# Kernel tuning notes

Hardware: AMD Instinct MI355X
Metric: run time of the kernel (lower is better)

The kernel has to match this reference:

```python
import jax, jax.numpy as jnp
import numpy as np

N = 50000
E = 800000
IN_C, HID, OUT_C = 512, 256, 128


def gcn_conv(x, edge_index, W, b, num_nodes):
    # PyG GCNConv: add self-loops, symmetric normalization, linear-then-aggregate.
    h = x @ W  # [N, out]
    src = jnp.concatenate([edge_index[0], jnp.arange(num_nodes)])
    dst = jnp.concatenate([edge_index[1], jnp.arange(num_nodes)])
    ones = jnp.ones(src.shape[0], dtype=x.dtype)
    deg = jax.ops.segment_sum(ones, dst, num_segments=num_nodes)  # in-degree incl. self-loop
    dinv = jax.lax.rsqrt(deg)  # deg >= 1 thanks to self-loops
    norm = dinv[src] * dinv[dst]  # [E+N]
    msg = h[src] * norm[:, None]  # gather + scale
    out = jax.ops.segment_sum(msg, dst, num_segments=num_nodes)  # scatter-add
    return out + b


def setup_inputs() -> dict:
    key = jax.random.key(0)
    k_x, k_e, k_w1, k_b1, k_w2, k_b2 = jax.random.split(key, 6)
    x = jax.random.normal(k_x, (N, IN_C), dtype=jnp.float32)
    edge_index = jax.random.randint(k_e, (2, E), 0, N, dtype=jnp.int64)
    s1 = 1.0 / np.sqrt(IN_C)
    s2 = 1.0 / np.sqrt(HID)
    W1 = jax.random.uniform(k_w1, (IN_C, HID), jnp.float32, -s1, s1)
    b1 = jax.random.uniform(k_b1, (HID,), jnp.float32, -s1, s1)
    W2 = jax.random.uniform(k_w2, (HID, OUT_C), jnp.float32, -s2, s2)
    b2 = jax.random.uniform(k_b2, (OUT_C,), jnp.float32, -s2, s2)
    return {"x": x, "edge_index": edge_index, "W1": W1, "b1": b1, "W2": W2, "b2": b2}


def reference(x, edge_index, W1, b1, W2, b2):
    h = gcn_conv(x, edge_index, W1, b1, N)
    h = jax.nn.relu(h)
    # dropout in eval mode == identity
    return gcn_conv(h, edge_index, W2, b2, N)
```

## Files before the change

### kernel.cpp

```cpp
#include <hip/hip_runtime.h>
#include <stdint.h>

typedef __bf16 bf16_t;
typedef bf16_t bf16x8 __attribute__((ext_vector_type(8)));
typedef bf16_t bf16x4 __attribute__((ext_vector_type(4)));
typedef bf16_t bf16x2 __attribute__((ext_vector_type(2)));
typedef float  f32x4  __attribute__((ext_vector_type(4)));

typedef __attribute__((address_space(3))) void* as3p;
typedef const __attribute__((address_space(1))) void* as1p;

#define IN_C 512
#define HID  256
#define OUTC 128

__global__ void k_prep(const float* __restrict__ x, const float* __restrict__ W1,
                       const float* __restrict__ W2, const void* __restrict__ ei,
                       int* __restrict__ flag, int* __restrict__ cnt,
                       bf16_t* __restrict__ Xb, bf16_t* __restrict__ W1t,
                       bf16_t* __restrict__ W2t, int n, int mpad) {
  int t = blockIdx.x * blockDim.x + threadIdx.x;
  const int NC = mpad * 64;
  if (t < NC) {
    int r = t >> 6, c8 = t & 63;
    bf16x8 o;
    if (r < n) {
      const float4* px = (const float4*)(x + (size_t)r * IN_C);
      float4 a = px[c8 * 2];
      float4 b = px[c8 * 2 + 1];
      o[0] = (bf16_t)a.x; o[1] = (bf16_t)a.y; o[2] = (bf16_t)a.z; o[3] = (bf16_t)a.w;
      o[4] = (bf16_t)b.x; o[5] = (bf16_t)b.y; o[6] = (bf16_t)b.z; o[7] = (bf16_t)b.w;
    } else {
      for (int i = 0; i < 8; ++i) o[i] = (bf16_t)0.0f;
    }
    *(bf16x8*)(Xb + (size_t)r * IN_C + c8 * 8) = o;
    return;
  }
  int u = t - NC;
  if (u < IN_C * HID) {
    W1t[(size_t)(u & 255) * IN_C + (u >> 8)] = (bf16_t)W1[u];
    return;
  }
  u -= IN_C * HID;
  if (u < HID * OUTC) {
    W2t[(size_t)(u & 127) * HID + (u >> 7)] = (bf16_t)W2[u];
    return;
  }
  u -= HID * OUTC;
  if (u < n) {
    cnt[u] = 0;
    return;
  }
  if (u == n) {
    const long long* p = (const long long*)ei;
    int ok = 1;
    for (int i = 0; i < 64; ++i) {
      long long v = p[i];
      if (v < 0 || v >= n) ok = 0;
    }
    *flag = ok;
  }
}

__global__ void k_hist(const void* __restrict__ ei, const int* __restrict__ flag,
                       int* __restrict__ cnt, int E) {
  int e = blockIdx.x * blockDim.x + threadIdx.x;
  if (e >= E) return;
  int d;
  if (*flag) d = (int)((const long long*)ei)[(size_t)E + e];
  else       d = ((const int*)ei)[E + e];
  atomicAdd(&cnt[d], 1);
}

__global__ void k_scan1(const int* __restrict__ cnt, int* __restrict__ ex,
                        int* __restrict__ part, float* __restrict__ dinv, int n) {
  __shared__ int sh[256];
  int i = blockIdx.x * 256 + threadIdx.x;
  int v = (i < n) ? cnt[i] : 0;
  if (i < n) dinv[i] = rsqrtf((float)v + 1.0f);
  sh[threadIdx.x] = v;
  __syncthreads();
  int val = v;
  for (int off = 1; off < 256; off <<= 1) {
    int t = (threadIdx.x >= off) ? sh[threadIdx.x - off] : 0;
    __syncthreads();
    val += t;
    sh[threadIdx.x] = val;
    __syncthreads();
  }
  if (i < n) ex[i] = val - v;
  if (threadIdx.x == 255) part[blockIdx.x] = val;
}

__global__ void k_scan23(int* __restrict__ rs, const int* __restrict__ part,
                         int* __restrict__ cur, int n, int Etot) {
  __shared__ int sh[256];
  const int b = blockIdx.x, t = threadIdx.x;
  int p = 0;
  for (int j = t; j < b; j += 256) p += part[j];
  sh[t] = p;
  __syncthreads();
  for (int off = 128; off > 0; off >>= 1) {
    if (t < off) sh[t] += sh[t + off];
    __syncthreads();
  }
  int base = sh[0];
  int i = b * 256 + t;
  if (i < n) {
    int r = rs[i] + base;
    rs[i] = r;
    cur[i] = r;
  }
  if (i == 0) rs[n] = Etot;
}

__global__ void k_fill(const void* __restrict__ ei, const int* __restrict__ flag,
                       int* __restrict__ cur, int2* __restrict__ csrw,
                       const float* __restrict__ dinv, int E) {
  int e = blockIdx.x * blockDim.x + threadIdx.x;
  if (e >= E) return;
  int s, d;
  if (*flag) {
    const long long* p = (const long long*)ei;
    s = (int)p[e];
    d = (int)p[(size_t)E + e];
  } else {
    const int* p = (const int*)ei;
    s = p[e];
    d = p[E + e];
  }
  int pos = atomicAdd(&cur[d], 1);
  int2 v;
  v.x = s;
  v.y = __float_as_int(dinv[s]);
  csrw[pos] = v;
}

__global__ __launch_bounds__(256, 3) void k_gemm(const bf16_t* __restrict__ A,
                                                 const bf16_t* __restrict__ Bt,
                                                 bf16_t* __restrict__ C,
                                                 int Kdim, int Ncols) {
  __shared__ bf16_t As[128 * 32];
  __shared__ bf16_t Bs[128 * 32];
  const int bm = blockIdx.x, bn = blockIdx.y;
  const int tid = threadIdx.x;
  const int wave = tid >> 6, lane = tid & 63;
  const int wm = (wave >> 1) * 64, wn = (wave & 1) * 64;
  const int quad = lane >> 4, l16 = lane & 15;

  const size_t abase = (size_t)bm * 128 * Kdim;
  const size_t bbase = (size_t)bn * 128 * Kdim;

  f32x4 acc[4][4];
#pragma unroll
  for (int i = 0; i < 4; ++i)
#pragma unroll
    for (int j = 0; j < 4; ++j)
#pragma unroll
      for (int r = 0; r < 4; ++r) acc[i][j][r] = 0.0f;

  for (int kk = 0; kk < Kdim; kk += 32) {
#pragma unroll
    for (int i = 0; i < 2; ++i) {
      int g = i * 256 + tid;
      int row = g >> 2, col = (g & 3) * 8;
      const bf16_t* ga = A + abase + (size_t)row * Kdim + kk + col;
      __builtin_amdgcn_global_load_lds((as1p)ga,
                                       (as3p)(&As[(i * 256 + wave * 64) * 8]), 16, 0, 0);
      const bf16_t* gb = Bt + bbase + (size_t)row * Kdim + kk + col;
      __builtin_amdgcn_global_load_lds((as1p)gb,
                                       (as3p)(&Bs[(i * 256 + wave * 64) * 8]), 16, 0, 0);
    }
    __syncthreads();
    bf16x8 af[4], bf[4];
#pragma unroll
    for (int i = 0; i < 4; ++i)
      af[i] = *(const bf16x8*)(&As[(wm + i * 16 + l16) * 32 + quad * 8]);
#pragma unroll
    for (int j = 0; j < 4; ++j)
      bf[j] = *(const bf16x8*)(&Bs[(wn + j * 16 + l16) * 32 + quad * 8]);
#pragma unroll
    for (int i = 0; i < 4; ++i)
#pragma unroll
      for (int j = 0; j < 4; ++j)
        acc[i][j] = __builtin_amdgcn_mfma_f32_16x16x32_bf16(af[i], bf[j], acc[i][j], 0, 0, 0);
    __syncthreads();
  }

#pragma unroll
  for (int i = 0; i < 4; ++i) {
#pragma unroll
    for (int j = 0; j < 4; ++j) {
      int col = bn * 128 + wn + j * 16 + l16;
      int row0 = bm * 128 + wm + i * 16 + quad * 4;
#pragma unroll
      for (int r = 0; r < 4; ++r)
        C[(size_t)(row0 + r) * Ncols + col] = (bf16_t)acc[i][j][r];
    }
  }
}

__global__ void k_agg_l1(const bf16_t* __restrict__ H, const int* __restrict__ rs,
                         const int2* __restrict__ csrw, const float* __restrict__ dinv,
                         const float* __restrict__ b1, bf16_t* __restrict__ R,
                         int n, int mpad) {
  int d = blockIdx.x * 4 + (threadIdx.x >> 6);
  if (d >= mpad) return;
  int lane = threadIdx.x & 63;
  if (d >= n) {
    bf16x4 z;
    z[0] = (bf16_t)0.0f; z[1] = (bf16_t)0.0f; z[2] = (bf16_t)0.0f; z[3] = (bf16_t)0.0f;
    *(bf16x4*)(R + (size_t)d * HID + lane * 4) = z;
    return;
  }
  int e0 = rs[d], e1 = rs[d + 1];
  float acc[4][4];
  for (int k = 0; k < 4; ++k)
    for (int c = 0; c < 4; ++c) acc[k][c] = 0.f;
  int e = e0;
  for (; e + 8 <= e1; e += 8) {
    int2 cw[8];
    bf16x4 h[8];
#pragma unroll
    for (int u = 0; u < 8; ++u) cw[u] = csrw[e + u];
#pragma unroll
    for (int u = 0; u < 8; ++u)
      h[u] = *(const bf16x4*)(H + (size_t)cw[u].x * HID + lane * 4);
#pragma unroll
    for (int u = 0; u < 8; ++u) {
      float w = __int_as_float(cw[u].y);
#pragma unroll
      for (int c = 0; c < 4; ++c) acc[u & 3][c] += w * (float)h[u][c];
    }
  }
  for (; e < e1; ++e) {
    int2 cw = csrw[e];
    float w = __int_as_float(cw.y);
    bf16x4 hx = *(const bf16x4*)(H + (size_t)cw.x * HID + lane * 4);
#pragma unroll
    for (int c = 0; c < 4; ++c) acc[0][c] += w * (float)hx[c];
  }
  float dd = dinv[d];
  float dv2 = dd * dd;
  bf16x4 hs = *(const bf16x4*)(H + (size_t)d * HID + lane * 4);
  float4 bb = ((const float4*)b1)[lane];
  float a0 = (acc[0][0] + acc[1][0]) + (acc[2][0] + acc[3][0]);
  float a1 = (acc[0][1] + acc[1][1]) + (acc[2][1] + acc[3][1]);
  float a2 = (acc[0][2] + acc[1][2]) + (acc[2][2] + acc[3][2]);
  float a3 = (acc[0][3] + acc[1][3]) + (acc[2][3] + acc[3][3]);
  float v0 = fmaxf(a0 * dd + dv2 * (float)hs[0] + bb.x, 0.f);
  float v1 = fmaxf(a1 * dd + dv2 * (float)hs[1] + bb.y, 0.f);
  float v2 = fmaxf(a2 * dd + dv2 * (float)hs[2] + bb.z, 0.f);
  float v3 = fmaxf(a3 * dd + dv2 * (float)hs[3] + bb.w, 0.f);
  bf16x4 o;
  o[0] = (bf16_t)v0; o[1] = (bf16_t)v1; o[2] = (bf16_t)v2; o[3] = (bf16_t)v3;
  *(bf16x4*)(R + (size_t)d * HID + lane * 4) = o;
}

__global__ void k_agg_l2(const bf16_t* __restrict__ H, const int* __restrict__ rs,
                         const int2* __restrict__ csrw, const float* __restrict__ dinv,
                         const float* __restrict__ b2, float* __restrict__ out, int n) {
  int d = blockIdx.x * 4 + (threadIdx.x >> 6);
  if (d >= n) return;
  int lane = threadIdx.x & 63;
  int e0 = rs[d], e1 = rs[d + 1];
  float acc[4][2];
  for (int k = 0; k < 4; ++k) { acc[k][0] = 0.f; acc[k][1] = 0.f; }
  int e = e0;
  for (; e + 8 <= e1; e += 8) {
    int2 cw[8];
    bf16x2 h[8];
#pragma unroll
    for (int u = 0; u < 8; ++u) cw[u] = csrw[e + u];
#pragma unroll
    for (int u = 0; u < 8; ++u)
      h[u] = *(const bf16x2*)(H + (size_t)cw[u].x * OUTC + lane * 2);
#pragma unroll
    for (int u = 0; u < 8; ++u) {
      float w = __int_as_float(cw[u].y);
      acc[u & 3][0] += w * (float)h[u][0];
      acc[u & 3][1] += w * (float)h[u][1];
    }
  }
  for (; e < e1; ++e) {
    int2 cw = csrw[e];
    float w = __int_as_float(cw.y);
    bf16x2 hx = *(const bf16x2*)(H + (size_t)cw.x * OUTC + lane * 2);
    acc[0][0] += w * (float)hx[0];
    acc[0][1] += w * (float)hx[1];
  }
  float a0 = (acc[0][0] + acc[1][0]) + (acc[2][0] + acc[3][0]);
  float a1 = (acc[0][1] + acc[1][1]) + (acc[2][1] + acc[3][1]);
  float dd = dinv[d];
  float dv2 = dd * dd;
  bf16x2 hs = *(const bf16x2*)(H + (size_t)d * OUTC + lane * 2);
  float2 bb = ((const float2*)b2)[lane];
  float2 o;
  o.x = a0 * dd + dv2 * (float)hs[0] + bb.x;
  o.y = a1 * dd + dv2 * (float)hs[1] + bb.y;
  ((float2*)(out + (size_t)d * OUTC))[lane] = o;
}

extern "C" void kernel_launch(void* const* d_in, const int* in_sizes, int n_in,
                              void* d_out, int out_size, void* d_ws, size_t ws_size,
                              hipStream_t stream) {
  const float* x  = (const float*)d_in[0];
  const void*  ei = d_in[1];
  const float* W1 = (const float*)d_in[2];
  const float* b1 = (const float*)d_in[3];
  const float* W2 = (const float*)d_in[4];
  const float* b2 = (const float*)d_in[5];

  const int n = in_sizes[0] / IN_C;
  const int E = in_sizes[1] / 2;
  const int mpad = (n + 127) & ~127;

  char* w = (char*)d_ws;
  size_t off = 0;
  auto alloc = [&](size_t bytes) -> void* {
    void* p = w + off;
    off = (off + bytes + 255) & ~(size_t)255;
    return p;
  };

  int*    flag = (int*)alloc(4);
  int*    cnt  = (int*)alloc((size_t)n * 4);
  float*  dinv = (float*)alloc((size_t)n * 4);
  int*    rs   = (int*)alloc((size_t)(n + 1) * 4);
  int*    cur  = (int*)alloc((size_t)n * 4);
  int*    part = (int*)alloc(1024);
  int2*   csrw = (int2*)alloc((size_t)E * 8);
  bf16_t* Xb   = (bf16_t*)alloc((size_t)mpad * IN_C * 2);
  bf16_t* W1t  = (bf16_t*)alloc((size_t)HID * IN_C * 2);
  bf16_t* W2t  = (bf16_t*)alloc((size_t)OUTC * HID * 2);
  bf16_t* H1b  = (bf16_t*)alloc((size_t)mpad * HID * 2);
  bf16_t* R1b  = (bf16_t*)alloc((size_t)mpad * HID * 2);
  bf16_t* H2b  = (bf16_t*)alloc((size_t)mpad * OUTC * 2);
  (void)ws_size; (void)n_in; (void)out_size;

  const int nb = (n + 255) / 256;
  const int prepT = mpad * 64 + IN_C * HID + HID * OUTC + n + 1;

  k_prep<<<(prepT + 255) / 256, 256, 0, stream>>>(x, W1, W2, ei, flag, cnt,
                                                  Xb, W1t, W2t, n, mpad);
  k_hist<<<(E + 255) / 256, 256, 0, stream>>>(ei, flag, cnt, E);
  k_scan1<<<nb, 256, 0, stream>>>(cnt, rs, part, dinv, n);
  k_scan23<<<nb, 256, 0, stream>>>(rs, part, cur, n, E);
  k_fill<<<(E + 255) / 256, 256, 0, stream>>>(ei, flag, cur, csrw, dinv, E);

  k_gemm<<<dim3(mpad / 128, HID / 128), 256, 0, stream>>>(Xb, W1t, H1b, IN_C, HID);
  k_agg_l1<<<(mpad + 3) / 4, 256, 0, stream>>>(H1b, rs, csrw, dinv, b1, R1b, n, mpad);
  k_gemm<<<dim3(mpad / 128, OUTC / 128), 256, 0, stream>>>(R1b, W2t, H2b, HID, OUTC);
  k_agg_l2<<<(n + 3) / 4, 256, 0, stream>>>(H2b, rs, csrw, dinv, b2, (float*)d_out, n);
}
```

Measured before the change: 397.0 us.

## Fuse fp32-to-bf16 conversion into layer-1 GEMM, merge scans, shrink CSR entries

The separate pass that converts x to bf16 is removed. The layer-1 GEMM now reads fp32 x directly, converts it in registers and stages it into padded LDS tiles, with each block covering the full 256 output columns. The two scan kernels become one, where each block recomputes its prefix by summing the preceding counts directly. CSR entries drop from (src, weight) pairs to plain src indices, and the aggregation kernels gather dinv[src] per edge instead. The trade-offs are redundant prefix summation work, extra random dinv loads in aggregation, and loss of the async global-to-LDS loads in GEMM1 along with lower occupancy.

```diff
diff --git a/kernel.cpp b/kernel.cpp
--- a/kernel.cpp
+++ b/kernel.cpp
@@ -14,29 +14,18 @@
 #define HID  256
 #define OUTC 128
 
-__global__ void k_prep(const float* __restrict__ x, const float* __restrict__ W1,
-                       const float* __restrict__ W2, const void* __restrict__ ei,
-                       int* __restrict__ flag, int* __restrict__ cnt,
-                       bf16_t* __restrict__ Xb, bf16_t* __restrict__ W1t,
-                       bf16_t* __restrict__ W2t, int n, int mpad) {
-  int t = blockIdx.x * blockDim.x + threadIdx.x;
-  const int NC = mpad * 64;
-  if (t < NC) {
-    int r = t >> 6, c8 = t & 63;
-    bf16x8 o;
-    if (r < n) {
-      const float4* px = (const float4*)(x + (size_t)r * IN_C);
-      float4 a = px[c8 * 2];
-      float4 b = px[c8 * 2 + 1];
-      o[0] = (bf16_t)a.x; o[1] = (bf16_t)a.y; o[2] = (bf16_t)a.z; o[3] = (bf16_t)a.w;
-      o[4] = (bf16_t)b.x; o[5] = (bf16_t)b.y; o[6] = (bf16_t)b.z; o[7] = (bf16_t)b.w;
-    } else {
-      for (int i = 0; i < 8; ++i) o[i] = (bf16_t)0.0f;
-    }
-    *(bf16x8*)(Xb + (size_t)r * IN_C + c8 * 8) = o;
-    return;
-  }
-  int u = t - NC;
+__device__ inline bf16x8 cvt8(float4 a, float4 b) {
+  bf16x8 o;
+  o[0] = (bf16_t)a.x; o[1] = (bf16_t)a.y; o[2] = (bf16_t)a.z; o[3] = (bf16_t)a.w;
+  o[4] = (bf16_t)b.x; o[5] = (bf16_t)b.y; o[6] = (bf16_t)b.z; o[7] = (bf16_t)b.w;
+  return o;
+}
+
+__global__ void k_prep(const float* __restrict__ W1, const float* __restrict__ W2,
+                       const void* __restrict__ ei, int* __restrict__ flag,
+                       int* __restrict__ cnt, bf16_t* __restrict__ W1t,
+                       bf16_t* __restrict__ W2t, int n) {
+  int u = blockIdx.x * blockDim.x + threadIdx.x;
   if (u < IN_C * HID) {
     W1t[(size_t)(u & 255) * IN_C + (u >> 8)] = (bf16_t)W1[u];
     return;
@@ -72,32 +61,13 @@
   atomicAdd(&cnt[d], 1);
 }
 
-__global__ void k_scan1(const int* __restrict__ cnt, int* __restrict__ ex,
-                        int* __restrict__ part, float* __restrict__ dinv, int n) {
-  __shared__ int sh[256];
-  int i = blockIdx.x * 256 + threadIdx.x;
-  int v = (i < n) ? cnt[i] : 0;
-  if (i < n) dinv[i] = rsqrtf((float)v + 1.0f);
-  sh[threadIdx.x] = v;
-  __syncthreads();
-  int val = v;
-  for (int off = 1; off < 256; off <<= 1) {
-    int t = (threadIdx.x >= off) ? sh[threadIdx.x - off] : 0;
-    __syncthreads();
-    val += t;
-    sh[threadIdx.x] = val;
-    __syncthreads();
-  }
-  if (i < n) ex[i] = val - v;
-  if (threadIdx.x == 255) part[blockIdx.x] = val;
-}
-
-__global__ void k_scan23(int* __restrict__ rs, const int* __restrict__ part,
-                         int* __restrict__ cur, int n, int Etot) {
+__global__ void k_scan(const int* __restrict__ cnt, int* __restrict__ rs,
+                       int* __restrict__ cur, float* __restrict__ dinv,
+                       int n, int Etot) {
   __shared__ int sh[256];
   const int b = blockIdx.x, t = threadIdx.x;
   int p = 0;
-  for (int j = t; j < b; j += 256) p += part[j];
+  for (int j = t; j < b * 256; j += 256) p += cnt[j];
   sh[t] = p;
   __syncthreads();
   for (int off = 128; off > 0; off >>= 1) {
@@ -105,9 +75,22 @@
     __syncthreads();
   }
   int base = sh[0];
+  __syncthreads();
   int i = b * 256 + t;
+  int v = (i < n) ? cnt[i] : 0;
+  if (i < n) dinv[i] = rsqrtf((float)v + 1.0f);
+  sh[t] = v;
+  __syncthreads();
+  int val = v;
+  for (int off = 1; off < 256; off <<= 1) {
+    int tt = (t >= off) ? sh[t - off] : 0;
+    __syncthreads();
+    val += tt;
+    sh[t] = val;
+    __syncthreads();
+  }
   if (i < n) {
-    int r = rs[i] + base;
+    int r = base + val - v;
     rs[i] = r;
     cur[i] = r;
   }
@@ -115,8 +98,7 @@
 }
 
 __global__ void k_fill(const void* __restrict__ ei, const int* __restrict__ flag,
-                       int* __restrict__ cur, int2* __restrict__ csrw,
-                       const float* __restrict__ dinv, int E) {
+                       int* __restrict__ cur, int* __restrict__ csr, int E) {
   int e = blockIdx.x * blockDim.x + threadIdx.x;
   if (e >= E) return;
   int s, d;
@@ -130,26 +112,91 @@
     d = p[E + e];
   }
   int pos = atomicAdd(&cur[d], 1);
-  int2 v;
-  v.x = s;
-  v.y = __float_as_int(dinv[s]);
-  csrw[pos] = v;
-}
-
-__global__ __launch_bounds__(256, 3) void k_gemm(const bf16_t* __restrict__ A,
-                                                 const bf16_t* __restrict__ Bt,
-                                                 bf16_t* __restrict__ C,
-                                                 int Kdim, int Ncols) {
+  csr[pos] = s;
+}
+
+__global__ __launch_bounds__(256, 2) void k_gemm1(const float* __restrict__ x,
+                                                  const bf16_t* __restrict__ W1t,
+                                                  bf16_t* __restrict__ C, int n) {
+  __shared__ bf16_t As[128 * 40];
+  __shared__ bf16_t Bs[256 * 40];
+  const int bm = blockIdx.x;
+  const int tid = threadIdx.x;
+  const int wave = tid >> 6, lane = tid & 63;
+  const int wm = (wave >> 1) * 64, wn = (wave & 1) * 128;
+  const int quad = lane >> 4, l16 = lane & 15;
+  const int arow = tid >> 1, acol = (tid & 1) * 16;
+  const int grow = bm * 128 + arow;
+  const bool av = grow < n;
+  const float* ap = x + (size_t)grow * IN_C + acol;
+  const bf16_t* bp = W1t + (size_t)tid * IN_C;
+
+  f32x4 acc[4][8];
+#pragma unroll
+  for (int i = 0; i < 4; ++i)
+#pragma unroll
+    for (int j = 0; j < 8; ++j)
+#pragma unroll
+      for (int r = 0; r < 4; ++r) acc[i][j][r] = 0.0f;
+
+  for (int kk = 0; kk < IN_C; kk += 32) {
+    float4 z = {0, 0, 0, 0};
+    float4 a0 = av ? *(const float4*)(ap + kk)      : z;
+    float4 a1 = av ? *(const float4*)(ap + kk + 4)  : z;
+    float4 a2 = av ? *(const float4*)(ap + kk + 8)  : z;
+    float4 a3 = av ? *(const float4*)(ap + kk + 12) : z;
+    bf16x8 vb0 = *(const bf16x8*)(bp + kk);
+    bf16x8 vb1 = *(const bf16x8*)(bp + kk + 8);
+    bf16x8 vb2 = *(const bf16x8*)(bp + kk + 16);
+    bf16x8 vb3 = *(const bf16x8*)(bp + kk + 24);
+    bf16x8 va0 = cvt8(a0, a1);
+    bf16x8 va1 = cvt8(a2, a3);
+    __syncthreads();
+    *(bf16x8*)(&As[arow * 40 + acol]) = va0;
+    *(bf16x8*)(&As[arow * 40 + acol + 8]) = va1;
+    *(bf16x8*)(&Bs[tid * 40]) = vb0;
+    *(bf16x8*)(&Bs[tid * 40 + 8]) = vb1;
+    *(bf16x8*)(&Bs[tid * 40 + 16]) = vb2;
+    *(bf16x8*)(&Bs[tid * 40 + 24]) = vb3;
+    __syncthreads();
+    bf16x8 af[4], bf[8];
+#pragma unroll
+    for (int i = 0; i < 4; ++i)
+      af[i] = *(const bf16x8*)(&As[(wm + i * 16 + l16) * 40 + quad * 8]);
+#pragma unroll
+    for (int j = 0; j < 8; ++j)
+      bf[j] = *(const bf16x8*)(&Bs[(wn + j * 16 + l16) * 40 + quad * 8]);
+#pragma unroll
+    for (int i = 0; i < 4; ++i)
+#pragma unroll
+      for (int j = 0; j < 8; ++j)
+        acc[i][j] = __builtin_amdgcn_mfma_f32_16x16x32_bf16(af[i], bf[j], acc[i][j], 0, 0, 0);
+  }
+
+#pragma unroll
+  for (int i = 0; i < 4; ++i) {
+#pragma unroll
+    for (int j = 0; j < 8; ++j) {
+      int col = wn + j * 16 + l16;
+      int row0 = bm * 128 + wm + i * 16 + quad * 4;
+#pragma unroll
+      for (int r = 0; r < 4; ++r)
+        C[(size_t)(row0 + r) * HID + col] = (bf16_t)acc[i][j][r];
+    }
+  }
+}
+
+__global__ __launch_bounds__(256, 3) void k_gemm2(const bf16_t* __restrict__ A,
+                                                  const bf16_t* __restrict__ Bt,
+                                                  bf16_t* __restrict__ C) {
   __shared__ bf16_t As[128 * 32];
   __shared__ bf16_t Bs[128 * 32];
-  const int bm = blockIdx.x, bn = blockIdx.y;
+  const int bm = blockIdx.x;
   const int tid = threadIdx.x;
   const int wave = tid >> 6, lane = tid & 63;
   const int wm = (wave >> 1) * 64, wn = (wave & 1) * 64;
   const int quad = lane >> 4, l16 = lane & 15;
-
-  const size_t abase = (size_t)bm * 128 * Kdim;
-  const size_t bbase = (size_t)bn * 128 * Kdim;
+  const size_t abase = (size_t)bm * 128 * HID;
 
   f32x4 acc[4][4];
 #pragma unroll
@@ -159,15 +206,15 @@
 #pragma unroll
       for (int r = 0; r < 4; ++r) acc[i][j][r] = 0.0f;
 
-  for (int kk = 0; kk < Kdim; kk += 32) {
+  for (int kk = 0; kk < HID; kk += 32) {
 #pragma unroll
     for (int i = 0; i < 2; ++i) {
       int g = i * 256 + tid;
       int row = g >> 2, col = (g & 3) * 8;
-      const bf16_t* ga = A + abase + (size_t)row * Kdim + kk + col;
+      const bf16_t* ga = A + abase + (size_t)row * HID + kk + col;
       __builtin_amdgcn_global_load_lds((as1p)ga,
                                        (as3p)(&As[(i * 256 + wave * 64) * 8]), 16, 0, 0);
-      const bf16_t* gb = Bt + bbase + (size_t)row * Kdim + kk + col;
+      const bf16_t* gb = Bt + (size_t)row * HID + kk + col;
       __builtin_amdgcn_global_load_lds((as1p)gb,
                                        (as3p)(&Bs[(i * 256 + wave * 64) * 8]), 16, 0, 0);
     }
@@ -191,17 +238,17 @@
   for (int i = 0; i < 4; ++i) {
 #pragma unroll
     for (int j = 0; j < 4; ++j) {
-      int col = bn * 128 + wn + j * 16 + l16;
+      int col = wn + j * 16 + l16;
       int row0 = bm * 128 + wm + i * 16 + quad * 4;
 #pragma unroll
       for (int r = 0; r < 4; ++r)
-        C[(size_t)(row0 + r) * Ncols + col] = (bf16_t)acc[i][j][r];
+        C[(size_t)(row0 + r) * OUTC + col] = (bf16_t)acc[i][j][r];
     }
   }
 }
 
 __global__ void k_agg_l1(const bf16_t* __restrict__ H, const int* __restrict__ rs,
-                         const int2* __restrict__ csrw, const float* __restrict__ dinv,
+                         const int* __restrict__ csr, const float* __restrict__ dinv,
                          const float* __restrict__ b1, bf16_t* __restrict__ R,
                          int n, int mpad) {
   int d = blockIdx.x * 4 + (threadIdx.x >> 6);
@@ -219,26 +266,27 @@
     for (int c = 0; c < 4; ++c) acc[k][c] = 0.f;
   int e = e0;
   for (; e + 8 <= e1; e += 8) {
-    int2 cw[8];
+    int s[8];
+    float w[8];
     bf16x4 h[8];
 #pragma unroll
-    for (int u = 0; u < 8; ++u) cw[u] = csrw[e + u];
+    for (int u = 0; u < 8; ++u) s[u] = csr[e + u];
+#pragma unroll
+    for (int u = 0; u < 8; ++u) w[u] = dinv[s[u]];
 #pragma unroll
     for (int u = 0; u < 8; ++u)
-      h[u] = *(const bf16x4*)(H + (size_t)cw[u].x * HID + lane * 4);
-#pragma unroll
-    for (int u = 0; u < 8; ++u) {
-      float w = __int_as_float(cw[u].y);
-#pragma unroll
-      for (int c = 0; c < 4; ++c) acc[u & 3][c] += w * (float)h[u][c];
-    }
+      h[u] = *(const bf16x4*)(H + (size_t)s[u] * HID + lane * 4);
+#pragma unroll
+    for (int u = 0; u < 8; ++u)
+#pragma unroll
+      for (int c = 0; c < 4; ++c) acc[u & 3][c] += w[u] * (float)h[u][c];
   }
   for (; e < e1; ++e) {
-    int2 cw = csrw[e];
-    float w = __int_as_float(cw.y);
-    bf16x4 hx = *(const bf16x4*)(H + (size_t)cw.x * HID + lane * 4);
-#pragma unroll
-    for (int c = 0; c < 4; ++c) acc[0][c] += w * (float)hx[c];
+    int sx = csr[e];
+    float wx = dinv[sx];
+    bf16x4 hx = *(const bf16x4*)(H + (size_t)sx * HID + lane * 4);
+#pragma unroll
+    for (int c = 0; c < 4; ++c) acc[0][c] += wx * (float)hx[c];
   }
   float dd = dinv[d];
   float dv2 = dd * dd;
@@ -258,7 +306,7 @@
 }
 
 __global__ void k_agg_l2(const bf16_t* __restrict__ H, const int* __restrict__ rs,
-                         const int2* __restrict__ csrw, const float* __restrict__ dinv,
+                         const int* __restrict__ csr, const float* __restrict__ dinv,
                          const float* __restrict__ b2, float* __restrict__ out, int n) {
   int d = blockIdx.x * 4 + (threadIdx.x >> 6);
   if (d >= n) return;
@@ -268,26 +316,28 @@
   for (int k = 0; k < 4; ++k) { acc[k][0] = 0.f; acc[k][1] = 0.f; }
   int e = e0;
   for (; e + 8 <= e1; e += 8) {
-    int2 cw[8];
+    int s[8];
+    float w[8];
     bf16x2 h[8];
 #pragma unroll
-    for (int u = 0; u < 8; ++u) cw[u] = csrw[e + u];
+    for (int u = 0; u < 8; ++u) s[u] = csr[e + u];
+#pragma unroll
+    for (int u = 0; u < 8; ++u) w[u] = dinv[s[u]];
 #pragma unroll
     for (int u = 0; u < 8; ++u)
-      h[u] = *(const bf16x2*)(H + (size_t)cw[u].x * OUTC + lane * 2);
+      h[u] = *(const bf16x2*)(H + (size_t)s[u] * OUTC + lane * 2);
 #pragma unroll
     for (int u = 0; u < 8; ++u) {
-      float w = __int_as_float(cw[u].y);
-      acc[u & 3][0] += w * (float)h[u][0];
-      acc[u & 3][1] += w * (float)h[u][1];
+      acc[u & 3][0] += w[u] * (float)h[u][0];
+      acc[u & 3][1] += w[u] * (float)h[u][1];
     }
   }
   for (; e < e1; ++e) {
-    int2 cw = csrw[e];
-    float w = __int_as_float(cw.y);
-    bf16x2 hx = *(const bf16x2*)(H + (size_t)cw.x * OUTC + lane * 2);
-    acc[0][0] += w * (float)hx[0];
-    acc[0][1] += w * (float)hx[1];
+    int sx = csr[e];
+    float wx = dinv[sx];
+    bf16x2 hx = *(const bf16x2*)(H + (size_t)sx * OUTC + lane * 2);
+    acc[0][0] += wx * (float)hx[0];
+    acc[0][1] += wx * (float)hx[1];
   }
   float a0 = (acc[0][0] + acc[1][0]) + (acc[2][0] + acc[3][0]);
   float a1 = (acc[0][1] + acc[1][1]) + (acc[2][1] + acc[3][1]);
@@ -328,9 +378,7 @@
   float*  dinv = (float*)alloc((size_t)n * 4);
   int*    rs   = (int*)alloc((size_t)(n + 1) * 4);
   int*    cur  = (int*)alloc((size_t)n * 4);
-  int*    part = (int*)alloc(1024);
-  int2*   csrw = (int2*)alloc((size_t)E * 8);
-  bf16_t* Xb   = (bf16_t*)alloc((size_t)mpad * IN_C * 2);
+  int*    csr  = (int*)alloc((size_t)E * 4);
   bf16_t* W1t  = (bf16_t*)alloc((size_t)HID * IN_C * 2);
   bf16_t* W2t  = (bf16_t*)alloc((size_t)OUTC * HID * 2);
   bf16_t* H1b  = (bf16_t*)alloc((size_t)mpad * HID * 2);
@@ -339,17 +387,15 @@
   (void)ws_size; (void)n_in; (void)out_size;
 
   const int nb = (n + 255) / 256;
-  const int prepT = mpad * 64 + IN_C * HID + HID * OUTC + n + 1;
-
-  k_prep<<<(prepT + 255) / 256, 256, 0, stream>>>(x, W1, W2, ei, flag, cnt,
-                                                  Xb, W1t, W2t, n, mpad);
+  const int prepT = IN_C * HID + HID * OUTC + n + 1;
+
+  k_prep<<<(prepT + 255) / 256, 256, 0, stream>>>(W1, W2, ei, flag, cnt, W1t, W2t, n);
   k_hist<<<(E + 255) / 256, 256, 0, stream>>>(ei, flag, cnt, E);
-  k_scan1<<<nb, 256, 0, stream>>>(cnt, rs, part, dinv, n);
-  k_scan23<<<nb, 256, 0, stream>>>(rs, part, cur, n, E);
-  k_fill<<<(E + 255) / 256, 256, 0, stream>>>(ei, flag, cur, csrw, dinv, E);
-
-  k_gemm<<<dim3(mpad / 128, HID / 128), 256, 0, stream>>>(Xb, W1t, H1b, IN_C, HID);
-  k_agg_l1<<<(mpad + 3) / 4, 256, 0, stream>>>(H1b, rs, csrw, dinv, b1, R1b, n, mpad);
-  k_gemm<<<dim3(mpad / 128, OUTC / 128), 256, 0, stream>>>(R1b, W2t, H2b, HID, OUTC);
-  k_agg_l2<<<(n + 3) / 4, 256, 0, stream>>>(H2b, rs, csrw, dinv, b2, (float*)d_out, n);
-}
+  k_scan<<<nb, 256, 0, stream>>>(cnt, rs, cur, dinv, n, E);
+  k_fill<<<(E + 255) / 256, 256, 0, stream>>>(ei, flag, cur, csr, E);
+
+  k_gemm1<<<mpad / 128, 256, 0, stream>>>(x, W1t, H1b, n);
+  k_agg_l1<<<(mpad + 3) / 4, 256, 0, stream>>>(H1b, rs, csr, dinv, b1, R1b, n, mpad);
+  k_gemm2<<<mpad / 128, 256, 0, stream>>>(R1b, W2t, H2b);
+  k_agg_l2<<<(n + 3) / 4, 256, 0, stream>>>(H2b, rs, csr, dinv, b2, (float*)d_out, n);
+}
```

New measurement: 454.9 us. +14.6%, slower.

## Merge scan kernels and store source-only CSR, gathering dinv in aggregation

Applied to the files above, without the earlier changes.

Folds the two-pass prefix scan into a single kernel in which each block recomputes its base offset by summing all preceding counts directly. The CSR now stores only source indices (int) rather than (src, dinv) pairs, which halves CSR bytes and lets the fill kernel skip the dinv gather. The aggregation kernels then gather dinv[s] per edge themselves. In exchange, each scan block does work that grows with its index (quadratic total reads of cnt), and aggregation picks up an extra dependent random load per edge.

```diff
diff --git a/kernel.cpp b/kernel.cpp
--- a/kernel.cpp
+++ b/kernel.cpp
@@ -72,32 +72,13 @@
   atomicAdd(&cnt[d], 1);
 }
 
-__global__ void k_scan1(const int* __restrict__ cnt, int* __restrict__ ex,
-                        int* __restrict__ part, float* __restrict__ dinv, int n) {
-  __shared__ int sh[256];
-  int i = blockIdx.x * 256 + threadIdx.x;
-  int v = (i < n) ? cnt[i] : 0;
-  if (i < n) dinv[i] = rsqrtf((float)v + 1.0f);
-  sh[threadIdx.x] = v;
-  __syncthreads();
-  int val = v;
-  for (int off = 1; off < 256; off <<= 1) {
-    int t = (threadIdx.x >= off) ? sh[threadIdx.x - off] : 0;
-    __syncthreads();
-    val += t;
-    sh[threadIdx.x] = val;
-    __syncthreads();
-  }
-  if (i < n) ex[i] = val - v;
-  if (threadIdx.x == 255) part[blockIdx.x] = val;
-}
-
-__global__ void k_scan23(int* __restrict__ rs, const int* __restrict__ part,
-                         int* __restrict__ cur, int n, int Etot) {
+__global__ void k_scan(const int* __restrict__ cnt, int* __restrict__ rs,
+                       int* __restrict__ cur, float* __restrict__ dinv,
+                       int n, int Etot) {
   __shared__ int sh[256];
   const int b = blockIdx.x, t = threadIdx.x;
   int p = 0;
-  for (int j = t; j < b; j += 256) p += part[j];
+  for (int j = t; j < b * 256; j += 256) p += cnt[j];
   sh[t] = p;
   __syncthreads();
   for (int off = 128; off > 0; off >>= 1) {
@@ -105,9 +86,22 @@
     __syncthreads();
   }
   int base = sh[0];
+  __syncthreads();
   int i = b * 256 + t;
+  int v = (i < n) ? cnt[i] : 0;
+  if (i < n) dinv[i] = rsqrtf((float)v + 1.0f);
+  sh[t] = v;
+  __syncthreads();
+  int val = v;
+  for (int off = 1; off < 256; off <<= 1) {
+    int tt = (t >= off) ? sh[t - off] : 0;
+    __syncthreads();
+    val += tt;
+    sh[t] = val;
+    __syncthreads();
+  }
   if (i < n) {
-    int r = rs[i] + base;
+    int r = base + val - v;
     rs[i] = r;
     cur[i] = r;
   }
@@ -115,8 +109,7 @@
 }
 
 __global__ void k_fill(const void* __restrict__ ei, const int* __restrict__ flag,
-                       int* __restrict__ cur, int2* __restrict__ csrw,
-                       const float* __restrict__ dinv, int E) {
+                       int* __restrict__ cur, int* __restrict__ csr, int E) {
   int e = blockIdx.x * blockDim.x + threadIdx.x;
   if (e >= E) return;
   int s, d;
@@ -130,10 +123,7 @@
     d = p[E + e];
   }
   int pos = atomicAdd(&cur[d], 1);
-  int2 v;
-  v.x = s;
-  v.y = __float_as_int(dinv[s]);
-  csrw[pos] = v;
+  csr[pos] = s;
 }
 
 __global__ __launch_bounds__(256, 3) void k_gemm(const bf16_t* __restrict__ A,
@@ -201,7 +191,7 @@
 }
 
 __global__ void k_agg_l1(const bf16_t* __restrict__ H, const int* __restrict__ rs,
-                         const int2* __restrict__ csrw, const float* __restrict__ dinv,
+                         const int* __restrict__ csr, const float* __restrict__ dinv,
                          const float* __restrict__ b1, bf16_t* __restrict__ R,
                          int n, int mpad) {
   int d = blockIdx.x * 4 + (threadIdx.x >> 6);
@@ -219,26 +209,27 @@
     for (int c = 0; c < 4; ++c) acc[k][c] = 0.f;
   int e = e0;
   for (; e + 8 <= e1; e += 8) {
-    int2 cw[8];
+    int s[8];
+    float w[8];
     bf16x4 h[8];
 #pragma unroll
-    for (int u = 0; u < 8; ++u) cw[u] = csrw[e + u];
+    for (int u = 0; u < 8; ++u) s[u] = csr[e + u];
+#pragma unroll
+    for (int u = 0; u < 8; ++u) w[u] = dinv[s[u]];
 #pragma unroll
     for (int u = 0; u < 8; ++u)
-      h[u] = *(const bf16x4*)(H + (size_t)cw[u].x * HID + lane * 4);
-#pragma unroll
-    for (int u = 0; u < 8; ++u) {
-      float w = __int_as_float(cw[u].y);
-#pragma unroll
-      for (int c = 0; c < 4; ++c) acc[u & 3][c] += w * (float)h[u][c];
-    }
+      h[u] = *(const bf16x4*)(H + (size_t)s[u] * HID + lane * 4);
+#pragma unroll
+    for (int u = 0; u < 8; ++u)
+#pragma unroll
+      for (int c = 0; c < 4; ++c) acc[u & 3][c] += w[u] * (float)h[u][c];
   }
   for (; e < e1; ++e) {
-    int2 cw = csrw[e];
-    float w = __int_as_float(cw.y);
-    bf16x4 hx = *(const bf16x4*)(H + (size_t)cw.x * HID + lane * 4);
-#pragma unroll
-    for (int c = 0; c < 4; ++c) acc[0][c] += w * (float)hx[c];
+    int sx = csr[e];
+    float wx = dinv[sx];
+    bf16x4 hx = *(const bf16x4*)(H + (size_t)sx * HID + lane * 4);
+#pragma unroll
+    for (int c = 0; c < 4; ++c) acc[0][c] += wx * (float)hx[c];
   }
   float dd = dinv[d];
   float dv2 = dd * dd;
@@ -258,7 +249,7 @@
 }
 
 __global__ void k_agg_l2(const bf16_t* __restrict__ H, const int* __restrict__ rs,
-                         const int2* __restrict__ csrw, const float* __restrict__ dinv,
+                         const int* __restrict__ csr, const float* __restrict__ dinv,
                          const float* __restrict__ b2, float* __restrict__ out, int n) {
   int d = blockIdx.x * 4 + (threadIdx.x >> 6);
   if (d >= n) return;
@@ -268,26 +259,28 @@
   for (int k = 0; k < 4; ++k) { acc[k][0] = 0.f; acc[k][1] = 0.f; }
   int e = e0;
   for (; e + 8 <= e1; e += 8) {
-    int2 cw[8];
+    int s[8];
+    float w[8];
     bf16x2 h[8];
 #pragma unroll
-    for (int u = 0; u < 8; ++u) cw[u] = csrw[e + u];
+    for (int u = 0; u < 8; ++u) s[u] = csr[e + u];
+#pragma unroll
+    for (int u = 0; u < 8; ++u) w[u] = dinv[s[u]];
 #pragma unroll
     for (int u = 0; u < 8; ++u)
-      h[u] = *(const bf16x2*)(H + (size_t)cw[u].x * OUTC + lane * 2);
+      h[u] = *(const bf16x2*)(H + (size_t)s[u] * OUTC + lane * 2);
 #pragma unroll
     for (int u = 0; u < 8; ++u) {
-      float w = __int_as_float(cw[u].y);
-      acc[u & 3][0] += w * (float)h[u][0];
-      acc[u & 3][1] += w * (float)h[u][1];
+      acc[u & 3][0] += w[u] * (float)h[u][0];
+      acc[u & 3][1] += w[u] * (float)h[u][1];
     }
   }
   for (; e < e1; ++e) {
-    int2 cw = csrw[e];
-    float w = __int_as_float(cw.y);
-    bf16x2 hx = *(const bf16x2*)(H + (size_t)cw.x * OUTC + lane * 2);
-    acc[0][0] += w * (float)hx[0];
-    acc[0][1] += w * (float)hx[1];
+    int sx = csr[e];
+    float wx = dinv[sx];
+    bf16x2 hx = *(const bf16x2*)(H + (size_t)sx * OUTC + lane * 2);
+    acc[0][0] += wx * (float)hx[0];
+    acc[0][1] += wx * (float)hx[1];
   }
   float a0 = (acc[0][0] + acc[1][0]) + (acc[2][0] + acc[3][0]);
   float a1 = (acc[0][1] + acc[1][1]) + (acc[2][1] + acc[3][1]);
@@ -328,8 +321,7 @@
   float*  dinv = (float*)alloc((size_t)n * 4);
   int*    rs   = (int*)alloc((size_t)(n + 1) * 4);
   int*    cur  = (int*)alloc((size_t)n * 4);
-  int*    part = (int*)alloc(1024);
-  int2*   csrw = (int2*)alloc((size_t)E * 8);
+  int*    csr  = (int*)alloc((size_t)E * 4);
   bf16_t* Xb   = (bf16_t*)alloc((size_t)mpad * IN_C * 2);
   bf16_t* W1t  = (bf16_t*)alloc((size_t)HID * IN_C * 2);
   bf16_t* W2t  = (bf16_t*)alloc((size_t)OUTC * HID * 2);
@@ -344,12 +336,11 @@
   k_prep<<<(prepT + 255) / 256, 256, 0, stream>>>(x, W1, W2, ei, flag, cnt,
                                                   Xb, W1t, W2t, n, mpad);
   k_hist<<<(E + 255) / 256, 256, 0, stream>>>(ei, flag, cnt, E);
-  k_scan1<<<nb, 256, 0, stream>>>(cnt, rs, part, dinv, n);
-  k_scan23<<<nb, 256, 0, stream>>>(rs, part, cur, n, E);
-  k_fill<<<(E + 255) / 256, 256, 0, stream>>>(ei, flag, cur, csrw, dinv, E);
+  k_scan<<<nb, 256, 0, stream>>>(cnt, rs, cur, dinv, n, E);
+  k_fill<<<(E + 255) / 256, 256, 0, stream>>>(ei, flag, cur, csr, E);
 
   k_gemm<<<dim3(mpad / 128, HID / 128), 256, 0, stream>>>(Xb, W1t, H1b, IN_C, HID);
-  k_agg_l1<<<(mpad + 3) / 4, 256, 0, stream>>>(H1b, rs, csrw, dinv, b1, R1b, n, mpad);
+  k_agg_l1<<<(mpad + 3) / 4, 256, 0, stream>>>(H1b, rs, csr, dinv, b1, R1b, n, mpad);
   k_gemm<<<dim3(mpad / 128, OUTC / 128), 256, 0, stream>>>(R1b, W2t, H2b, HID, OUTC);
-  k_agg_l2<<<(n + 3) / 4, 256, 0, stream>>>(H2b, rs, csrw, dinv, b2, (float*)d_out, n);
-}
+  k_agg_l2<<<(n + 3) / 4, 256, 0, stream>>>(H2b, rs, csr, dinv, b2, (float*)d_out, n);
+}
```

New measurement: 426.6 us. +7.4%, slower.
